# Performance work log

Hardware: AMD Instinct MI355X
Metric: run time of the kernel (lower is better)

Reference implementation:

```python
import jax, jax.numpy as jnp
import numpy as np

N = 4096
IN_F = 256
OUT_F = 64
HEADS = 8
ALPHA = 0.2  # LeakyReLU negative slope


def setup_inputs() -> dict:
    key = jax.random.key(0)
    k1, k2, k3, k4 = jax.random.split(key, 4)
    X = jax.random.normal(k1, (N, IN_F), dtype=jnp.float32)
    adj = jax.random.randint(k2, (N, N), 0, 2, dtype=jnp.int32)
    # self-loops so every row has at least one neighbor (softmax well-defined)
    idx = jnp.arange(N)
    adj = adj.at[idx, idx].set(1)
    W = jax.random.normal(k3, (HEADS, IN_F, OUT_F), dtype=jnp.float32) * 0.05
    a = jax.random.normal(k4, (HEADS, 2 * OUT_F, 1), dtype=jnp.float32) * 0.05
    return {"X": X, "adj": adj, "W": W, "a": a}


def reference(X, adj, W, a):
    # H: [heads, N, F]
    H = jnp.einsum('ni,hio->hno', X, W)
    F_ = H.shape[-1]
    # cat([h_i, h_j]) @ a  ==  h_i @ a[:F] + h_j @ a[F:]
    a1 = a[:, :F_, 0]   # [heads, F]
    a2 = a[:, F_:, 0]   # [heads, F]
    f1 = jnp.einsum('hnf,hf->hn', H, a1)  # score contribution of row node i
    f2 = jnp.einsum('hnf,hf->hn', H, a2)  # score contribution of col node j
    e = jax.nn.leaky_relu(f1[:, :, None] + f2[:, None, :], negative_slope=ALPHA)  # [heads, N, N]
    e = jnp.where(adj[None, :, :] == 0, -jnp.inf, e)
    attention = jax.nn.softmax(e, axis=-1)
    # dropout omitted (eval mode)
    H_out = jnp.einsum('hnm,hmf->hnf', attention, H)  # [heads, N, F]
    return H_out.mean(axis=0)  # [N, F]
```

## Files before the change

### kernel.cpp

```cpp
#include <hip/hip_runtime.h>
#include <hip/hip_bf16.h>

#define N_NODES 4096
#define IN_F 256
#define OUT_F 64
#define HEADS 8
#define ALPHA 0.2f

typedef _Float16 f16x8 __attribute__((ext_vector_type(8)));
typedef float f32x4 __attribute__((ext_vector_type(4)));
union U4 { uint4 u; f16x8 h; unsigned w[4]; };

#define WFRAG_OFF 0
#define BFRAG_OFF (WFRAG_OFF + 8*8*4*64*8*2)
#define F1_OFF    (BFRAG_OFF + 8*128*4*64*8*2)
#define GP_OFF    (F1_OFF + 8*4096*4)
#define GN_OFF    (GP_OFF + 8*4096*2)
#define ADJ_OFF   (GN_OFF + 8*4096*2)

static __device__ __forceinline__ unsigned pkmul(unsigned a, unsigned b) {
  unsigned r; asm("v_pk_mul_f16 %0, %1, %2" : "=v"(r) : "v"(a), "v"(b)); return r;
}
static __device__ __forceinline__ unsigned pkmax(unsigned a, unsigned b) {
  unsigned r; asm("v_pk_max_f16 %0, %1, %2" : "=v"(r) : "v"(a), "v"(b)); return r;
}
static __device__ __forceinline__ unsigned pkadd(unsigned a, unsigned b) {
  unsigned r; asm("v_pk_add_f16 %0, %1, %2" : "=v"(r) : "v"(a), "v"(b)); return r;
}
static __device__ __forceinline__ unsigned short f2h_bits(float f) {
  return __builtin_bit_cast(unsigned short, (_Float16)f);
}
static __device__ __forceinline__ float h2f(unsigned short x) {
  return (float)__builtin_bit_cast(_Float16, x);
}

__global__ __launch_bounds__(256) void k_pre(const float* __restrict__ W,
                                             _Float16* __restrict__ wfrag,
                                             float* __restrict__ out) {
  int b = blockIdx.x, t = threadIdx.x;
  if (b < 8) {
    int h = b;
    for (int pos = t; pos < 2048; pos += 256) {
      int kt = pos >> 8, ct = (pos >> 6) & 3, l = pos & 63;
      int lr = l & 15, lg = l >> 4;
#pragma unroll
      for (int e = 0; e < 8; ++e)
        wfrag[(size_t)(((h*8 + kt)*4 + ct)*64 + l) * 8 + e]
          = (_Float16)W[(size_t)(h*256 + kt*32 + lg*8 + e) * 64 + ct*16 + lr];
    }
  } else {
    float4* oz = ((float4*)out) + (size_t)(b - 8) * 8192;
    float4 zz = make_float4(0.f, 0.f, 0.f, 0.f);
    for (int q = t; q < 8192; q += 256) oz[q] = zz;
  }
}

__global__ __launch_bounds__(256) void k_main(
    const float* __restrict__ X, const int* __restrict__ adj,
    const _Float16* __restrict__ wfrag, const float* __restrict__ a,
    unsigned long long* __restrict__ bits, _Float16* __restrict__ bfrag,
    float* __restrict__ f1, _Float16* __restrict__ Gp, _Float16* __restrict__ Gn) {
  int b = blockIdx.x, t = threadIdx.x;
  if (b >= 512) {
    int b2 = b - 512;
    int lane = t & 63;
    int waveid = b2 * 4 + (t >> 6);
#pragma unroll
    for (int it2 = 0; it2 < 8; ++it2) {
      int w0 = waveid + (it2*4 + 0) * 8192;
      int w1 = waveid + (it2*4 + 1) * 8192;
      int w2 = waveid + (it2*4 + 2) * 8192;
      int w3 = waveid + (it2*4 + 3) * 8192;
      int v0 = __builtin_nontemporal_load(adj + (size_t)w0 * 64 + lane);
      int v1 = __builtin_nontemporal_load(adj + (size_t)w1 * 64 + lane);
      int v2 = __builtin_nontemporal_load(adj + (size_t)w2 * 64 + lane);
      int v3 = __builtin_nontemporal_load(adj + (size_t)w3 * 64 + lane);
      unsigned long long m0 = __ballot(v0 != 0);
      unsigned long long m1 = __ballot(v1 != 0);
      unsigned long long m2 = __ballot(v2 != 0);
      unsigned long long m3 = __ballot(v3 != 0);
      if (lane == 0) { bits[w0] = m0; bits[w1] = m1; bits[w2] = m2; bits[w3] = m3; }
    }
    return;
  }
  int h = b & 7, rb = b >> 3;
  int w = t >> 6, l = t & 63;
  int i0 = rb * 64 + w * 16;
  int r = l & 15, g = l >> 4;
  const U4* wv = (const U4*)wfrag;
  f32x4 z = {0.f, 0.f, 0.f, 0.f};
  f32x4 acc[4] = {z, z, z, z};
#pragma unroll
  for (int kt = 0; kt < 8; ++kt) {
    const float4* xr = (const float4*)(X + (size_t)(i0 + r) * 256 + (kt*4 + g) * 8);
    float4 x0 = xr[0], x1 = xr[1];
    U4 af;
    af.h[0] = (_Float16)x0.x; af.h[1] = (_Float16)x0.y;
    af.h[2] = (_Float16)x0.z; af.h[3] = (_Float16)x0.w;
    af.h[4] = (_Float16)x1.x; af.h[5] = (_Float16)x1.y;
    af.h[6] = (_Float16)x1.z; af.h[7] = (_Float16)x1.w;
#pragma unroll
    for (int ct = 0; ct < 4; ++ct) {
      U4 bv = wv[((h*8 + kt)*4 + ct)*64 + l];
      acc[ct] = __builtin_amdgcn_mfma_f32_16x16x32_f16(af.h, bv.h, acc[ct], 0, 0, 0);
    }
  }
  int jb = i0 + g*4;
#pragma unroll
  for (int ct = 0; ct < 4; ++ct) {
    size_t base = ((((size_t)h*128 + (jb>>5))*4 + ct)*64 + ((jb>>3)&3)*16 + r) * 8
                  + (jb & 7);
    union { short4 s; _Float16 hh[4]; } sv;
#pragma unroll
    for (int ri = 0; ri < 4; ++ri) sv.hh[ri] = (_Float16)acc[ct][ri];
    *(short4*)(bfrag + base) = sv.s;
  }
  float a1v[4], a2v[4];
#pragma unroll
  for (int ct = 0; ct < 4; ++ct) {
    a1v[ct] = a[h*128 + ct*16 + r];
    a2v[ct] = a[h*128 + 64 + ct*16 + r];
  }
#pragma unroll
  for (int ri = 0; ri < 4; ++ri) {
    float s1 = acc[0][ri]*a1v[0] + acc[1][ri]*a1v[1]
             + acc[2][ri]*a1v[2] + acc[3][ri]*a1v[3];
    float s2 = acc[0][ri]*a2v[0] + acc[1][ri]*a2v[1]
             + acc[2][ri]*a2v[2] + acc[3][ri]*a2v[3];
#pragma unroll
    for (int off = 1; off < 16; off <<= 1) {
      s1 += __shfl_xor(s1, off);
      s2 += __shfl_xor(s2, off);
    }
    if (r == 0) {
      int row = i0 + g*4 + ri;
      f1[h*4096 + row] = s1;
      Gp[h*4096 + row] = (_Float16)__expf(s2);
      Gn[h*4096 + row] = (_Float16)__expf(ALPHA * s2);
    }
  }
}

#define ATTN_BODY(PF, JT, DOPF) {                                              \
  U4 gp, gn;                                                                   \
  gp.u = Gs0[(JT)*4 + g].u;                                                    \
  gn.u = Gs1[(JT)*4 + g].u;                                                    \
  U4 b0, b1, b2, b3;                                                           \
  b0.u = PF[0]; b1.u = PF[1]; b2.u = PF[2]; b3.u = PF[3];                      \
  _Pragma("unroll")                                                            \
  for (int rg = 0; rg < 4; ++rg) {                                             \
    unsigned wm = Lb[rg*16 + r][JT];                                           \
    U4 av;                                                                     \
    _Pragma("unroll")                                                          \
    for (int p = 0; p < 4; ++p) {                                              \
      unsigned pm = pkmax(pkmul(Epp[rg], gp.w[p]), pkmul(Enn[rg], gn.w[p]));   \
      av.w[p] = pm & MLUT[(wm >> (g8 + 2*p)) & 3u];                            \
    }                                                                          \
    acc[rg][0] = __builtin_amdgcn_mfma_f32_16x16x32_f16(av.h, b0.h, acc[rg][0], 0,0,0); \
    acc[rg][1] = __builtin_amdgcn_mfma_f32_16x16x32_f16(av.h, b1.h, acc[rg][1], 0,0,0); \
    acc[rg][2] = __builtin_amdgcn_mfma_f32_16x16x32_f16(av.h, b2.h, acc[rg][2], 0,0,0); \
    acc[rg][3] = __builtin_amdgcn_mfma_f32_16x16x32_f16(av.h, b3.h, acc[rg][3], 0,0,0); \
    unsigned sden = pkadd(pkadd(av.w[0], av.w[1]), pkadd(av.w[2], av.w[3]));   \
    den[rg] += h2f((unsigned short)(sden & 0xFFFFu))                           \
             + h2f((unsigned short)(sden >> 16));                              \
  }                                                                            \
  if (DOPF) {                                                                  \
    _Pragma("unroll")                                                          \
    for (int c = 0; c < 4; ++c) PF[c] = bfh[((JT) + 2)*256 + c*64];            \
  }                                                                            \
}

#define WRBUF(i) {                                                             \
  _Pragma("unroll")                                                            \
  for (int rg = 0; rg < 4; ++rg)                                               \
    _Pragma("unroll")                                                          \
    for (int ct = 0; ct < 4; ++ct) redp[(i)*1088 + (rg*4+ct)*64 + l] = acc[rg][ct]; \
  f32x4 dv = {den[0], den[1], den[2], den[3]};                                 \
  redp[(i)*1088 + 1024 + l] = dv;                                              \
}
#define ADBUF(i) {                                                             \
  _Pragma("unroll")                                                            \
  for (int rg = 0; rg < 4; ++rg)                                               \
    _Pragma("unroll")                                                          \
    for (int ct = 0; ct < 4; ++ct) acc[rg][ct] += redp[(i)*1088 + (rg*4+ct)*64 + l]; \
  f32x4 dv = redp[(i)*1088 + 1024 + l];                                        \
  den[0] += dv[0]; den[1] += dv[1]; den[2] += dv[2]; den[3] += dv[3];          \
}

__global__ __launch_bounds__(256, 3) void k_attn(
    const float* __restrict__ f1, const unsigned int* __restrict__ adjbits,
    const _Float16* __restrict__ Gp, const _Float16* __restrict__ Gn,
    const _Float16* __restrict__ bfrag, float* __restrict__ out) {
  __shared__ __align__(16) char smem[49408];
  __shared__ unsigned MLUT[4];
  unsigned (*Lb)[129] = (unsigned(*)[129])smem;
  U4* Gs0 = (U4*)(smem + 33024);
  U4* Gs1 = (U4*)(smem + 41216);
  f32x4* redp = (f32x4*)smem;
  int b = blockIdx.x;
  int h = b & 7, rs = b >> 3;
  int i0 = rs * 64;
  int t = threadIdx.x, jq = t >> 6, l = t & 63;
  int r = l & 15, g = l >> 4, g8 = g * 8;
  if (t < 4) MLUT[t] = ((t & 1) ? 0xFFFFu : 0u) | ((t & 2) ? 0xFFFF0000u : 0u);
  const uint4* bfh = (const uint4*)bfrag + (size_t)h * 32768 + l;
  int jt0 = jq * 32;
  uint4 pA[4], pB[4];
#pragma unroll
  for (int c = 0; c < 4; ++c) pA[c] = bfh[jt0 * 256 + c*64];
#pragma unroll
  for (int c = 0; c < 4; ++c) pB[c] = bfh[(jt0 + 1) * 256 + c*64];
  for (int q = t; q < 8192; q += 256)
    Lb[q >> 7][q & 127] = adjbits[(size_t)(i0 + (q >> 7)) * 128 + (q & 127)];
  {
    const uint4* gp4 = (const uint4*)(Gp + (size_t)h * 4096);
    const uint4* gn4 = (const uint4*)(Gn + (size_t)h * 4096);
    for (int q = t; q < 512; q += 256) {
      Gs0[q].u = gp4[q];
      Gs1[q].u = gn4[q];
    }
  }
  unsigned Epp[4], Enn[4];
#pragma unroll
  for (int rg = 0; rg < 4; ++rg) {
    float f1r = f1[h * N_NODES + i0 + rg*16 + r];
    unsigned short ep = f2h_bits(__expf(f1r));
    unsigned short en = f2h_bits(__expf(ALPHA * f1r));
    Epp[rg] = ep | ((unsigned)ep << 16);
    Enn[rg] = en | ((unsigned)en << 16);
  }
  __syncthreads();
  f32x4 z = {0.f,0.f,0.f,0.f};
  f32x4 acc[4][4] = {{z,z,z,z},{z,z,z,z},{z,z,z,z},{z,z,z,z}};
  float den[4] = {0.f, 0.f, 0.f, 0.f};
  for (int q2 = 0; q2 < 16; ++q2) {
    ATTN_BODY(pA, jt0 + q2*2,     (q2 < 15));
    ATTN_BODY(pB, jt0 + q2*2 + 1, (q2 < 15));
  }
  __syncthreads();
  if (jq == 1) WRBUF(0);
  if (jq == 3) WRBUF(1);
  __syncthreads();
  if (jq == 0) ADBUF(0);
  if (jq == 2) ADBUF(1);
  __syncthreads();
  if (jq == 2) WRBUF(0);
  __syncthreads();
  if (jq == 0) {
    ADBUF(0);
#pragma unroll
    for (int rg = 0; rg < 4; ++rg) {
      den[rg] += __shfl_xor(den[rg], 16);
      den[rg] += __shfl_xor(den[rg], 32);
    }
#pragma unroll
    for (int rg = 0; rg < 4; ++rg)
#pragma unroll
      for (int ri = 0; ri < 4; ++ri) {
        float dr = __shfl(den[rg], g*4 + ri);
        float sc = 0.125f / dr;
        float* op = out + (size_t)(i0 + rg*16 + g*4 + ri) * 64;
        atomicAdd(op + r,      acc[rg][0][ri] * sc);
        atomicAdd(op + 16 + r, acc[rg][1][ri] * sc);
        atomicAdd(op + 32 + r, acc[rg][2][ri] * sc);
        atomicAdd(op + 48 + r, acc[rg][3][ri] * sc);
      }
  }
}

extern "C" void kernel_launch(void* const* d_in, const int* in_sizes, int n_in,
                              void* d_out, int out_size, void* d_ws, size_t ws_size,
                              hipStream_t stream) {
  const float* X = (const float*)d_in[0];
  const int* adj = (const int*)d_in[1];
  const float* W = (const float*)d_in[2];
  const float* a = (const float*)d_in[3];
  float* out = (float*)d_out;
  char* ws = (char*)d_ws;

  _Float16* wfrag = (_Float16*)(ws + WFRAG_OFF);
  _Float16* bfrag = (_Float16*)(ws + BFRAG_OFF);
  float* f1 = (float*)(ws + F1_OFF);
  _Float16* Gp = (_Float16*)(ws + GP_OFF);
  _Float16* Gn = (_Float16*)(ws + GN_OFF);
  unsigned long long* bits64 = (unsigned long long*)(ws + ADJ_OFF);
  const unsigned int* bits32 = (const unsigned int*)(ws + ADJ_OFF);

  k_pre<<<dim3(16), dim3(256), 0, stream>>>(W, wfrag, out);
  k_main<<<dim3(2560), dim3(256), 0, stream>>>(X, adj, wfrag, a, bits64, bfrag,
                                               f1, Gp, Gn);
  k_attn<<<dim3(512), dim3(256), 0, stream>>>(f1, bits32, Gp, Gn, bfrag, out);
}
```

Before: 74.69 us.

## Split attention rows across 8 waves and compute denominators via MFMA with ones

The attention kernel now launches 512 threads per block, with two row-halves each covered by four j-quarter waves. Each wave therefore holds half the accumulators and processes two 16-row groups instead of four. The softmax denominator is now accumulated by an extra MFMA against a ones column, replacing the packed f16 adds and scalar conversions, and the reduction buffers are resized to match. This aims to raise wave-level parallelism and cut VALU work per tile. The cost is one extra MFMA per row group and duplicate loads of the B fragments across the two row-halves.

```diff
diff --git a/kernel.cpp b/kernel.cpp
--- a/kernel.cpp
+++ b/kernel.cpp
@@ -24,14 +24,8 @@
 static __device__ __forceinline__ unsigned pkmax(unsigned a, unsigned b) {
   unsigned r; asm("v_pk_max_f16 %0, %1, %2" : "=v"(r) : "v"(a), "v"(b)); return r;
 }
-static __device__ __forceinline__ unsigned pkadd(unsigned a, unsigned b) {
-  unsigned r; asm("v_pk_add_f16 %0, %1, %2" : "=v"(r) : "v"(a), "v"(b)); return r;
-}
 static __device__ __forceinline__ unsigned short f2h_bits(float f) {
   return __builtin_bit_cast(unsigned short, (_Float16)f);
-}
-static __device__ __forceinline__ float h2f(unsigned short x) {
-  return (float)__builtin_bit_cast(_Float16, x);
 }
 
 __global__ __launch_bounds__(256) void k_pre(const float* __restrict__ W,
@@ -148,8 +142,8 @@
   U4 b0, b1, b2, b3;                                                           \
   b0.u = PF[0]; b1.u = PF[1]; b2.u = PF[2]; b3.u = PF[3];                      \
   _Pragma("unroll")                                                            \
-  for (int rg = 0; rg < 4; ++rg) {                                             \
-    unsigned wm = Lb[rg*16 + r][JT];                                           \
+  for (int rg = 0; rg < 2; ++rg) {                                             \
+    unsigned wm = Lb[rh32 + rg*16 + r][JT];                                    \
     U4 av;                                                                     \
     _Pragma("unroll")                                                          \
     for (int p = 0; p < 4; ++p) {                                              \
@@ -160,9 +154,7 @@
     acc[rg][1] = __builtin_amdgcn_mfma_f32_16x16x32_f16(av.h, b1.h, acc[rg][1], 0,0,0); \
     acc[rg][2] = __builtin_amdgcn_mfma_f32_16x16x32_f16(av.h, b2.h, acc[rg][2], 0,0,0); \
     acc[rg][3] = __builtin_amdgcn_mfma_f32_16x16x32_f16(av.h, b3.h, acc[rg][3], 0,0,0); \
-    unsigned sden = pkadd(pkadd(av.w[0], av.w[1]), pkadd(av.w[2], av.w[3]));   \
-    den[rg] += h2f((unsigned short)(sden & 0xFFFFu))                           \
-             + h2f((unsigned short)(sden >> 16));                              \
+    dn[rg]     = __builtin_amdgcn_mfma_f32_16x16x32_f16(av.h, bones.h, dn[rg], 0,0,0);  \
   }                                                                            \
   if (DOPF) {                                                                  \
     _Pragma("unroll")                                                          \
@@ -172,22 +164,20 @@
 
 #define WRBUF(i) {                                                             \
   _Pragma("unroll")                                                            \
-  for (int rg = 0; rg < 4; ++rg)                                               \
-    _Pragma("unroll")                                                          \
-    for (int ct = 0; ct < 4; ++ct) redp[(i)*1088 + (rg*4+ct)*64 + l] = acc[rg][ct]; \
-  f32x4 dv = {den[0], den[1], den[2], den[3]};                                 \
-  redp[(i)*1088 + 1024 + l] = dv;                                              \
-}
+  for (int rg = 0; rg < 2; ++rg) {                                             \
+    _Pragma("unroll")                                                          \
+    for (int ct = 0; ct < 4; ++ct) redp[(i)*640 + (rg*4+ct)*64 + l] = acc[rg][ct]; \
+    redp[(i)*640 + 512 + rg*64 + l] = dn[rg];                                  \
+  } }
 #define ADBUF(i) {                                                             \
   _Pragma("unroll")                                                            \
-  for (int rg = 0; rg < 4; ++rg)                                               \
-    _Pragma("unroll")                                                          \
-    for (int ct = 0; ct < 4; ++ct) acc[rg][ct] += redp[(i)*1088 + (rg*4+ct)*64 + l]; \
-  f32x4 dv = redp[(i)*1088 + 1024 + l];                                        \
-  den[0] += dv[0]; den[1] += dv[1]; den[2] += dv[2]; den[3] += dv[3];          \
-}
-
-__global__ __launch_bounds__(256, 3) void k_attn(
+  for (int rg = 0; rg < 2; ++rg) {                                             \
+    _Pragma("unroll")                                                          \
+    for (int ct = 0; ct < 4; ++ct) acc[rg][ct] += redp[(i)*640 + (rg*4+ct)*64 + l]; \
+    dn[rg] += redp[(i)*640 + 512 + rg*64 + l];                                 \
+  } }
+
+__global__ __launch_bounds__(512, 4) void k_attn(
     const float* __restrict__ f1, const unsigned int* __restrict__ adjbits,
     const _Float16* __restrict__ Gp, const _Float16* __restrict__ Gn,
     const _Float16* __restrict__ bfrag, float* __restrict__ out) {
@@ -200,7 +190,9 @@
   int b = blockIdx.x;
   int h = b & 7, rs = b >> 3;
   int i0 = rs * 64;
-  int t = threadIdx.x, jq = t >> 6, l = t & 63;
+  int t = threadIdx.x, wid = t >> 6, l = t & 63;
+  int rh = wid >> 2, jq = wid & 3;
+  int rh32 = rh * 32;
   int r = l & 15, g = l >> 4, g8 = g * 8;
   if (t < 4) MLUT[t] = ((t & 1) ? 0xFFFFu : 0u) | ((t & 2) ? 0xFFFF0000u : 0u);
   const uint4* bfh = (const uint4*)bfrag + (size_t)h * 32768 + l;
@@ -210,56 +202,46 @@
   for (int c = 0; c < 4; ++c) pA[c] = bfh[jt0 * 256 + c*64];
 #pragma unroll
   for (int c = 0; c < 4; ++c) pB[c] = bfh[(jt0 + 1) * 256 + c*64];
-  for (int q = t; q < 8192; q += 256)
+  for (int q = t; q < 8192; q += 512)
     Lb[q >> 7][q & 127] = adjbits[(size_t)(i0 + (q >> 7)) * 128 + (q & 127)];
-  {
-    const uint4* gp4 = (const uint4*)(Gp + (size_t)h * 4096);
-    const uint4* gn4 = (const uint4*)(Gn + (size_t)h * 4096);
-    for (int q = t; q < 512; q += 256) {
-      Gs0[q].u = gp4[q];
-      Gs1[q].u = gn4[q];
-    }
-  }
-  unsigned Epp[4], Enn[4];
-#pragma unroll
-  for (int rg = 0; rg < 4; ++rg) {
-    float f1r = f1[h * N_NODES + i0 + rg*16 + r];
+  Gs0[t].u = ((const uint4*)(Gp + (size_t)h * 4096))[t];
+  Gs1[t].u = ((const uint4*)(Gn + (size_t)h * 4096))[t];
+  unsigned Epp[2], Enn[2];
+#pragma unroll
+  for (int rg = 0; rg < 2; ++rg) {
+    float f1r = f1[h * N_NODES + i0 + rh32 + rg*16 + r];
     unsigned short ep = f2h_bits(__expf(f1r));
     unsigned short en = f2h_bits(__expf(ALPHA * f1r));
     Epp[rg] = ep | ((unsigned)ep << 16);
     Enn[rg] = en | ((unsigned)en << 16);
   }
+  unsigned ov = (r == 0) ? 0x3C003C00u : 0u;
+  U4 bones; bones.u = make_uint4(ov, ov, ov, ov);
   __syncthreads();
   f32x4 z = {0.f,0.f,0.f,0.f};
-  f32x4 acc[4][4] = {{z,z,z,z},{z,z,z,z},{z,z,z,z},{z,z,z,z}};
-  float den[4] = {0.f, 0.f, 0.f, 0.f};
+  f32x4 acc[2][4] = {{z,z,z,z},{z,z,z,z}};
+  f32x4 dn[2] = {z, z};
   for (int q2 = 0; q2 < 16; ++q2) {
     ATTN_BODY(pA, jt0 + q2*2,     (q2 < 15));
     ATTN_BODY(pB, jt0 + q2*2 + 1, (q2 < 15));
   }
   __syncthreads();
-  if (jq == 1) WRBUF(0);
-  if (jq == 3) WRBUF(1);
-  __syncthreads();
-  if (jq == 0) ADBUF(0);
-  if (jq == 2) ADBUF(1);
-  __syncthreads();
-  if (jq == 2) WRBUF(0);
+  if (jq == 1 || jq == 3) WRBUF(rh*2 + (jq >> 1));
+  __syncthreads();
+  if (jq == 0) ADBUF(rh*2);
+  if (jq == 2) ADBUF(rh*2 + 1);
+  __syncthreads();
+  if (jq == 2) WRBUF(rh);
   __syncthreads();
   if (jq == 0) {
-    ADBUF(0);
-#pragma unroll
-    for (int rg = 0; rg < 4; ++rg) {
-      den[rg] += __shfl_xor(den[rg], 16);
-      den[rg] += __shfl_xor(den[rg], 32);
-    }
-#pragma unroll
-    for (int rg = 0; rg < 4; ++rg)
+    ADBUF(rh);
+#pragma unroll
+    for (int rg = 0; rg < 2; ++rg)
 #pragma unroll
       for (int ri = 0; ri < 4; ++ri) {
-        float dr = __shfl(den[rg], g*4 + ri);
+        float dr = __shfl(dn[rg][ri], l & 48);
         float sc = 0.125f / dr;
-        float* op = out + (size_t)(i0 + rg*16 + g*4 + ri) * 64;
+        float* op = out + (size_t)(i0 + rh32 + rg*16 + g*4 + ri) * 64;
         atomicAdd(op + r,      acc[rg][0][ri] * sc);
         atomicAdd(op + 16 + r, acc[rg][1][ri] * sc);
         atomicAdd(op + 32 + r, acc[rg][2][ri] * sc);
@@ -289,5 +271,5 @@
   k_pre<<<dim3(16), dim3(256), 0, stream>>>(W, wfrag, out);
   k_main<<<dim3(2560), dim3(256), 0, stream>>>(X, adj, wfrag, a, bits64, bfrag,
                                                f1, Gp, Gn);
-  k_attn<<<dim3(512), dim3(256), 0, stream>>>(f1, bits32, Gp, Gn, bfrag, out);
-}
+  k_attn<<<dim3(512), dim3(512), 0, stream>>>(f1, bits32, Gp, Gn, bfrag, out);
+}
```

After: 71.93 us. -3.7%, faster.
